# Kernel tuning notes

Hardware: AMD Instinct MI355X
Metric: run time of the kernel (lower is better)

## Reference

```python
import jax, jax.numpy as jnp
import numpy as np

N, E, D, L, BOT = 50000, 800000, 64, 5, 15
EPS = 1e-5  # BatchNorm eps (torch default)
GATE = 0.01


def _bn(x, g, b):
    # training-mode BatchNorm1d over the node (batch) axis, biased variance
    m = jnp.mean(x, axis=0)
    v = jnp.mean((x - m) ** 2, axis=0)
    return (x - m) * jax.lax.rsqrt(v + EPS) * g + b


def _adapter(x, w1, b1, w2, b2, g, b):
    # Linear(D->BOT) -> ReLU -> Linear(BOT->D) -> BatchNorm1d
    h = jax.nn.relu(x @ w1 + b1)
    return _bn(h @ w2 + b2, g, b)


def setup_inputs() -> dict:
    key = jax.random.key(0)
    ks = jax.random.split(key, 8)
    x = jax.random.normal(ks[0], (N, D), dtype=jnp.float32)
    edge_index = jax.random.randint(ks[1], (2, E), 0, N, dtype=jnp.int32)
    # per-layer conv Linear weights
    W = jax.random.normal(ks[2], (L, D, D), dtype=jnp.float32) * 0.05
    b = jnp.zeros((L, D), dtype=jnp.float32)
    # per-layer output BatchNorm
    bn_g = jnp.ones((L, D), dtype=jnp.float32)
    bn_b = jnp.zeros((L, D), dtype=jnp.float32)
    # adapter branches: [prompt_num=2, L, ...] (random init so grads are nontrivial)
    pw1 = jax.random.normal(ks[3], (2, L, D, BOT), dtype=jnp.float32) * 0.1
    pb1 = jnp.zeros((2, L, BOT), dtype=jnp.float32)
    pw2 = jax.random.normal(ks[4], (2, L, BOT, D), dtype=jnp.float32) * 0.1
    pb2 = jnp.zeros((2, L, D), dtype=jnp.float32)
    pbn_g = jnp.ones((2, L, D), dtype=jnp.float32)
    pbn_b = jnp.zeros((2, L, D), dtype=jnp.float32)
    gating = jnp.full((2, L, 1), GATE, dtype=jnp.float32)
    return dict(x=x, edge_index=edge_index, W=W, b=b, bn_g=bn_g, bn_b=bn_b,
                pw1=pw1, pb1=pb1, pw2=pw2, pb2=pb2, pbn_g=pbn_g, pbn_b=pbn_b,
                gating=gating)


def reference(x, edge_index, W, b, bn_g, bn_b, pw1, pb1, pw2, pb2, pbn_g, pbn_b, gating):
    src, dst = edge_index[0], edge_index[1]
    h = x
    for l in range(L):
        # mess: sum-aggregate neighbor features (scatter-add over dst)
        x_aggr = jax.ops.segment_sum(h[src], dst, num_segments=N)  # [N, D]
        # conv: Linear on aggregated messages
        h_mlp = x_aggr @ W[l] + b[l]
        hn = _bn(h_mlp, bn_g[l], bn_b[l])
        # adapter branch 0 on layer input, branch 1 on aggregated messages
        hn = hn + _adapter(h, pw1[0, l], pb1[0, l], pw2[0, l], pb2[0, l], pbn_g[0, l], pbn_b[0, l]) * gating[0, l]
        hn = hn + _adapter(x_aggr, pw1[1, l], pb1[1, l], pw2[1, l], pb2[1, l], pbn_g[1, l], pbn_b[1, l]) * gating[1, l]
        if l < L - 1:
            hn = jax.nn.relu(hn)
        # dropout with drop_ratio=0 is a no-op
        h = hn
    return h
```

## Files before the change

### kernel.cpp

```cpp
#include <hip/hip_runtime.h>

#define DIM 64
#define BOT 15
#define NLAYERS 5
#define BN_EPS 1e-5f
#define ROWS 64
#define ROWS_FB 32
#define BKT_SHIFT 8

__device__ inline void fma4(float4& acc, const float4& a, float s) {
    acc.x = fmaf(a.x, s, acc.x); acc.y = fmaf(a.y, s, acc.y);
    acc.z = fmaf(a.z, s, acc.z); acc.w = fmaf(a.w, s, acc.w);
}
__device__ inline void add4(float4& acc, const float4& a) {
    acc.x += a.x; acc.y += a.y; acc.z += a.z; acc.w += a.w;
}
__device__ inline void fma4sq(float4& acc, const float4& a) {
    acc.x = fmaf(a.x, a.x, acc.x); acc.y = fmaf(a.y, a.y, acc.y);
    acc.z = fmaf(a.z, a.z, acc.z); acc.w = fmaf(a.w, a.w, acc.w);
}
__device__ inline void wavered4(float4& v) {
    v.x += __shfl_xor(v.x, 16); v.y += __shfl_xor(v.y, 16);
    v.z += __shfl_xor(v.z, 16); v.w += __shfl_xor(v.w, 16);
    v.x += __shfl_xor(v.x, 32); v.y += __shfl_xor(v.y, 32);
    v.z += __shfl_xor(v.z, 32); v.w += __shfl_xor(v.w, 32);
}


__global__ __launch_bounds__(256) void hist_k(const int* __restrict__ dst,
                                              int* __restrict__ deg, int E) {
    int e = blockIdx.x * blockDim.x + threadIdx.x;
    if (e < E) atomicAdd(&deg[dst[e]], 1);
}

__global__ __launch_bounds__(1024) void scan_part_k(const int* __restrict__ deg,
                                                    int* __restrict__ excl,
                                                    int* __restrict__ bsum, int n) {
    __shared__ int buf[1024];
    int t = threadIdx.x;
    int idx = blockIdx.x * 1024 + t;
    int v = (idx < n) ? deg[idx] : 0;
    buf[t] = v;
    __syncthreads();
    for (int off = 1; off < 1024; off <<= 1) {
        int x = (t >= off) ? buf[t - off] : 0;
        __syncthreads();
        buf[t] += x;
        __syncthreads();
    }
    if (idx < n) excl[idx] = buf[t] - v;
    if (t == 0) bsum[blockIdx.x] = buf[1023];
}

__global__ __launch_bounds__(1024) void scan_top_k(const int* __restrict__ bsum,
                                                   int* __restrict__ boff, int nb,
                                                   int* __restrict__ row_ptr, int n) {
    __shared__ int buf[1024];
    int t = threadIdx.x;
    int v = (t < nb) ? bsum[t] : 0;
    buf[t] = v;
    __syncthreads();
    for (int off = 1; off < 1024; off <<= 1) {
        int x = (t >= off) ? buf[t - off] : 0;
        __syncthreads();
        buf[t] += x;
        __syncthreads();
    }
    if (t < nb) boff[t] = buf[t] - v;
    if (t == 1023) row_ptr[n] = buf[1023];
}

__global__ __launch_bounds__(256) void scan_add_k(int* __restrict__ row_ptr,
                                                  const int* __restrict__ boff,
                                                  int* __restrict__ deg,
                                                  int* __restrict__ bcur, int n) {
    int i = blockIdx.x * blockDim.x + threadIdx.x;
    if (i < n) {
        int v = row_ptr[i] + boff[i >> 10];
        row_ptr[i] = v;
        deg[i] = v;
        if ((i & 255) == 0) bcur[i >> BKT_SHIFT] = v;
    }
}

__global__ __launch_bounds__(256) void scatter_k(const int* __restrict__ src,
                                                 const int* __restrict__ dst,
                                                 int* __restrict__ cursor,
                                                 int* __restrict__ csr, int E) {
    int e = blockIdx.x * blockDim.x + threadIdx.x;
    if (e < E) {
        int p = atomicAdd(&cursor[dst[e]], 1);
        csr[p] = src[e];
    }
}

__global__ __launch_bounds__(256) void part_k(const int* __restrict__ src,
                                              const int* __restrict__ dst,
                                              int* __restrict__ bcur,
                                              int2* __restrict__ part, int E) {
    __shared__ int hist[256];
    __shared__ int cur[256];
    int t = threadIdx.x;
    int base = blockIdx.x * 2048;
    hist[t] = 0;
    __syncthreads();
    int2 ed[8];
    int bk[8];
    #pragma unroll
    for (int k = 0; k < 8; k++) {
        int i = base + k * 256 + t;
        if (i < E) {
            ed[k].x = src[i];
            ed[k].y = dst[i];
            bk[k] = ed[k].y >> BKT_SHIFT;
            atomicAdd(&hist[bk[k]], 1);
        } else bk[k] = -1;
    }
    __syncthreads();
    int h = hist[t];
    if (h > 0) cur[t] = atomicAdd(&bcur[t], h);
    __syncthreads();
    #pragma unroll
    for (int k = 0; k < 8; k++) {
        if (bk[k] >= 0) {
            int p = atomicAdd(&cur[bk[k]], 1);
            part[p] = ed[k];
        }
    }
}

__global__ __launch_bounds__(256) void bscat_k(const int2* __restrict__ part,
                                               const int* __restrict__ row_ptr,
                                               int* __restrict__ cursor,
                                               int* __restrict__ csr, int n) {
    int b = blockIdx.x;
    int lo = row_ptr[b << BKT_SHIFT];
    int hiN = (b + 1) << BKT_SHIFT;
    int hi = row_ptr[hiN < n ? hiN : n];
    for (int i = lo + (int)threadIdx.x; i < hi; i += 256) {
        int2 e = part[i];
        int p = atomicAdd(&cursor[e.y], 1);
        csr[p] = e.x;
    }
}


__global__ __launch_bounds__(256) void aggr_k(const float* __restrict__ h,
                                              const int* __restrict__ row_ptr,
                                              const int* __restrict__ csr,
                                              float* __restrict__ out, int n) {
    int gid = blockIdx.x * blockDim.x + threadIdx.x;
    int node = gid >> 6;
    int lane = threadIdx.x & 63;
    if (node >= n) return;
    int j = lane >> 4, q = lane & 15;
    int s = row_ptr[node], e = row_ptr[node + 1];
    float4 acc = {0.f, 0.f, 0.f, 0.f};
    #pragma unroll 4
    for (int i = s; i < e; i += 4) {
        int ii = i + j;
        if (ii < e) {
            int idx = csr[ii];
            float4 v = *(const float4*)&h[(size_t)idx * DIM + q * 4];
            add4(acc, v);
        }
    }
    wavered4(acc);
    if (lane < 16) *(float4*)&out[(size_t)node * DIM + q * 4] = acc;
}


__global__ __launch_bounds__(512, 4) void stats_k(
    const float* __restrict__ h, const float* __restrict__ aggr,
    const float* __restrict__ Wc, const float* __restrict__ bc,
    const float* __restrict__ p1a, const float* __restrict__ b1a,
    const float* __restrict__ p2a, const float* __restrict__ b2a,
    const float* __restrict__ p1b, const float* __restrict__ b1b,
    const float* __restrict__ p2b, const float* __restrict__ b2b,
    float* __restrict__ partials,
    float* __restrict__ yv, float* __restrict__ uv, float* __restrict__ vv,
    int n) {
    __shared__ float xa_s[ROWS][68];
    __shared__ float wc_s[64][64];
    __shared__ float p1t_s[2][15][68];
    __shared__ float p2_s[2][15][64];
    __shared__ float m_s[2][ROWS][17];
    __shared__ float red_s[6][8][64];

    int t = threadIdx.x;
    int rowBase = blockIdx.x * ROWS;

    #pragma unroll
    for (int i = 0; i < 2; i++) {
        int idx = t + i * 512;
        int r = idx >> 4, c4 = (idx & 15) * 4;
        int gr = rowBase + r;
        float4 va = {0.f, 0.f, 0.f, 0.f};
        if (gr < n) va = *(const float4*)&aggr[(size_t)gr * DIM + c4];
        *(float4*)&xa_s[r][c4] = va;
    }
    #pragma unroll
    for (int i = 0; i < 2; i++) {
        int idx = t + i * 512;
        int k = idx >> 4, c4 = (idx & 15) * 4;
        *(float4*)&wc_s[k][c4] = *(const float4*)&Wc[k * DIM + c4];
    }
    if (t < 240) {
        int m = t >> 4, c4 = (t & 15) * 4;
        *(float4*)&p2_s[0][m][c4] = *(const float4*)&p2a[m * DIM + c4];
        *(float4*)&p2_s[1][m][c4] = *(const float4*)&p2b[m * DIM + c4];
    }
    #pragma unroll
    for (int i = 0; i < 2; i++) {
        int idx = t + i * 512;
        if (idx < 960) {
            int k = idx / 15, m = idx % 15;
            p1t_s[0][m][k] = p1a[idx];
            p1t_s[1][m][k] = p1b[idx];
        }
    }
    __syncthreads();

    {
        int m = t & 15, r2 = t >> 4;
        if (m < 15) {
            #pragma unroll
            for (int half = 0; half < 2; half++) {
                int r = r2 + half * 32;
                int gr = rowBase + r;
                if (gr < n) {
                    float sA = b1a[m], sB = b1b[m];
                    const float4* hp = (const float4*)&h[(size_t)gr * DIM];
                    #pragma unroll 4
                    for (int kq = 0; kq < 16; kq++) {
                        float4 hv = hp[kq];
                        float4 av = *(const float4*)&xa_s[r][kq * 4];
                        float4 wA = *(const float4*)&p1t_s[0][m][kq * 4];
                        float4 wB = *(const float4*)&p1t_s[1][m][kq * 4];
                        sA = fmaf(hv.x, wA.x, sA); sA = fmaf(hv.y, wA.y, sA);
                        sA = fmaf(hv.z, wA.z, sA); sA = fmaf(hv.w, wA.w, sA);
                        sB = fmaf(av.x, wB.x, sB); sB = fmaf(av.y, wB.y, sB);
                        sB = fmaf(av.z, wB.z, sB); sB = fmaf(av.w, wB.w, sB);
                    }
                    m_s[0][r][m] = fmaxf(sA, 0.f);
                    m_s[1][r][m] = fmaxf(sB, 0.f);
                } else {
                    m_s[0][r][m] = 0.f;
                    m_s[1][r][m] = 0.f;
                }
            }
        }
    }
    __syncthreads();

    int cg = t & 15, rg = t >> 4;
    int c0 = cg * 4;
    int r0 = rg, r1 = rg + 32;

    float4 s0 = *(const float4*)&bc[c0];
    float4 s1 = s0;
    #pragma unroll 4
    for (int kq = 0; kq < 16; kq++) {
        float4 w0 = *(const float4*)&wc_s[kq * 4 + 0][c0];
        float4 w1 = *(const float4*)&wc_s[kq * 4 + 1][c0];
        float4 w2 = *(const float4*)&wc_s[kq * 4 + 2][c0];
        float4 w3 = *(const float4*)&wc_s[kq * 4 + 3][c0];
        float4 a0 = *(const float4*)&xa_s[r0][kq * 4];
        float4 a1 = *(const float4*)&xa_s[r1][kq * 4];
        fma4(s0, w0, a0.x); fma4(s0, w1, a0.y); fma4(s0, w2, a0.z); fma4(s0, w3, a0.w);
        fma4(s1, w0, a1.x); fma4(s1, w1, a1.y); fma4(s1, w2, a1.z); fma4(s1, w3, a1.w);
    }

    float4 u0 = *(const float4*)&b2a[c0];
    float4 u1 = u0;
    float4 v0 = *(const float4*)&b2b[c0];
    float4 v1 = v0;
    #pragma unroll 5
    for (int m = 0; m < BOT; m++) {
        float4 wa = *(const float4*)&p2_s[0][m][c0];
        float4 wb = *(const float4*)&p2_s[1][m][c0];
        float a0 = m_s[0][r0][m], a1 = m_s[0][r1][m];
        float b0 = m_s[1][r0][m], b1 = m_s[1][r1][m];
        fma4(u0, wa, a0); fma4(u1, wa, a1);
        fma4(v0, wb, b0); fma4(v1, wb, b1);
    }

    float4 sy = {0,0,0,0}, sy2 = {0,0,0,0};
    float4 su = {0,0,0,0}, su2 = {0,0,0,0};
    float4 sv = {0,0,0,0}, sv2 = {0,0,0,0};
    {
        int gr = rowBase + r0;
        if (gr < n) {
            size_t o = (size_t)gr * DIM + c0;
            *(float4*)&yv[o] = s0; *(float4*)&uv[o] = u0; *(float4*)&vv[o] = v0;
            add4(sy, s0); fma4sq(sy2, s0);
            add4(su, u0); fma4sq(su2, u0);
            add4(sv, v0); fma4sq(sv2, v0);
        }
        gr = rowBase + r1;
        if (gr < n) {
            size_t o = (size_t)gr * DIM + c0;
            *(float4*)&yv[o] = s1; *(float4*)&uv[o] = u1; *(float4*)&vv[o] = v1;
            add4(sy, s1); fma4sq(sy2, s1);
            add4(su, u1); fma4sq(su2, u1);
            add4(sv, v1); fma4sq(sv2, v1);
        }
    }

    wavered4(sy); wavered4(sy2);
    wavered4(su); wavered4(su2);
    wavered4(sv); wavered4(sv2);

    int wv = t >> 6, lane = t & 63;
    if (lane < 16) {
        *(float4*)&red_s[0][wv][c0] = sy;
        *(float4*)&red_s[1][wv][c0] = sy2;
        *(float4*)&red_s[2][wv][c0] = su;
        *(float4*)&red_s[3][wv][c0] = su2;
        *(float4*)&red_s[4][wv][c0] = sv;
        *(float4*)&red_s[5][wv][c0] = sv2;
    }
    __syncthreads();
    if (t < DIM) {
        #pragma unroll
        for (int j = 0; j < 6; j++) {
            float v = red_s[j][0][t] + red_s[j][1][t] + red_s[j][2][t] + red_s[j][3][t]
                    + red_s[j][4][t] + red_s[j][5][t] + red_s[j][6][t] + red_s[j][7][t];
            partials[((size_t)blockIdx.x * 6 + j) * DIM + t] = v;
        }
    }
}


template <int RELU>
__global__ __launch_bounds__(256) void apply_k(
    const float* __restrict__ yv, const float* __restrict__ uv,
    const float* __restrict__ vv, const float* __restrict__ ST,
    float* __restrict__ out, int n4) {
    int i = blockIdx.x * blockDim.x + threadIdx.x;
    if (i >= n4) return;
    int c4 = (i & 15) * 4;
    float4 S0 = *(const float4*)&ST[c4];
    float4 T0 = *(const float4*)&ST[64 + c4];
    float4 S1 = *(const float4*)&ST[128 + c4];
    float4 T1 = *(const float4*)&ST[192 + c4];
    float4 S2 = *(const float4*)&ST[256 + c4];
    float4 T2 = *(const float4*)&ST[320 + c4];
    float4 y = *(const float4*)&yv[(size_t)i * 4];
    float4 u = *(const float4*)&uv[(size_t)i * 4];
    float4 v = *(const float4*)&vv[(size_t)i * 4];
    float4 r;
    r.x = fmaf(y.x, S0.x, T0.x) + fmaf(u.x, S1.x, T1.x) + fmaf(v.x, S2.x, T2.x);
    r.y = fmaf(y.y, S0.y, T0.y) + fmaf(u.y, S1.y, T1.y) + fmaf(v.y, S2.y, T2.y);
    r.z = fmaf(y.z, S0.z, T0.z) + fmaf(u.z, S1.z, T1.z) + fmaf(v.z, S2.z, T2.z);
    r.w = fmaf(y.w, S0.w, T0.w) + fmaf(u.w, S1.w, T1.w) + fmaf(v.w, S2.w, T2.w);
    if (RELU) {
        r.x = fmaxf(r.x, 0.f); r.y = fmaxf(r.y, 0.f);
        r.z = fmaxf(r.z, 0.f); r.w = fmaxf(r.w, 0.f);
    }
    *(float4*)&out[(size_t)i * 4] = r;
}


template <int MODE>
__global__ __launch_bounds__(256) void layer_k(
    const float* __restrict__ h, const float* __restrict__ aggr,
    const float* __restrict__ Wc, const float* __restrict__ bc,
    const float* __restrict__ p1a, const float* __restrict__ b1a,
    const float* __restrict__ p2a, const float* __restrict__ b2a,
    const float* __restrict__ p1b, const float* __restrict__ b1b,
    const float* __restrict__ p2b, const float* __restrict__ b2b,
    float* __restrict__ partials, const float* __restrict__ ST,
    float* __restrict__ hout, int n) {
    __shared__ float xh[ROWS_FB][DIM + 1];
    __shared__ float xa[ROWS_FB][DIM + 1];
    __shared__ float m0[ROWS_FB][17];
    __shared__ float m1[ROWS_FB][17];
    __shared__ float red[6][4][DIM];

    int t = threadIdx.x;
    int rowBase = blockIdx.x * ROWS_FB;

    #pragma unroll
    for (int i = 0; i < (ROWS_FB * DIM) / 256; i++) {
        int idx = t + i * 256;
        int r = idx >> 6, c = idx & 63;
        int gr = rowBase + r;
        float vh = 0.f, va = 0.f;
        if (gr < n) { vh = h[(size_t)gr * DIM + c]; va = aggr[(size_t)gr * DIM + c]; }
        xh[r][c] = vh;
        xa[r][c] = va;
    }
    __syncthreads();

    {
        int r = t >> 3, sub = t & 7;
        #pragma unroll
        for (int half = 0; half < 2; half++) {
            int m = sub + half * 8;
            if (m < BOT) {
                float s0 = b1a[m], s1 = b1b[m];
                #pragma unroll
                for (int k = 0; k < DIM; k++) {
                    s0 = fmaf(xh[r][k], p1a[k * BOT + m], s0);
                    s1 = fmaf(xa[r][k], p1b[k * BOT + m], s1);
                }
                m0[r][m] = fmaxf(s0, 0.f);
                m1[r][m] = fmaxf(s1, 0.f);
            }
        }
    }
    __syncthreads();

    int col = t & 63;
    int rg = t >> 6;
    float sums[6] = {0.f, 0.f, 0.f, 0.f, 0.f, 0.f};
    float S0 = 0, T0 = 0, S1 = 0, T1 = 0, S2 = 0, T2 = 0;
    if (MODE != 0) {
        S0 = ST[col];        T0 = ST[64 + col];
        S1 = ST[128 + col];  T1 = ST[192 + col];
        S2 = ST[256 + col];  T2 = ST[320 + col];
    }
    #pragma unroll
    for (int i = 0; i < ROWS_FB / 4; i++) {
        int r = rg + i * 4;
        int gr = rowBase + r;
        float s = bc[col];
        #pragma unroll
        for (int k = 0; k < DIM; k++) s = fmaf(xa[r][k], Wc[k * DIM + col], s);
        float u = b2a[col];
        #pragma unroll
        for (int m = 0; m < BOT; m++) u = fmaf(m0[r][m], p2a[m * DIM + col], u);
        float v = b2b[col];
        #pragma unroll
        for (int m = 0; m < BOT; m++) v = fmaf(m1[r][m], p2b[m * DIM + col], v);
        if (MODE == 0) {
            if (gr < n) {
                sums[0] += s; sums[1] += s * s;
                sums[2] += u; sums[3] += u * u;
                sums[4] += v; sums[5] += v * v;
            }
        } else {
            float r0 = fmaf(s, S0, T0) + fmaf(u, S1, T1) + fmaf(v, S2, T2);
            if (MODE == 2) r0 = fmaxf(r0, 0.f);
            if (gr < n) hout[(size_t)gr * DIM + col] = r0;
        }
    }

    if (MODE == 0) {
        #pragma unroll
        for (int j = 0; j < 6; j++) red[j][rg][col] = sums[j];
        __syncthreads();
        if (t < DIM) {
            #pragma unroll
            for (int j = 0; j < 6; j++) {
                float v = red[j][0][t] + red[j][1][t] + red[j][2][t] + red[j][3][t];
                partials[((size_t)blockIdx.x * 6 + j) * DIM + t] = v;
            }
        }
    }
}


__global__ __launch_bounds__(256) void reduce_fold_k(
    const float* __restrict__ partials, int nb, int n,
    const float* __restrict__ bn_g, const float* __restrict__ bn_b,
    const float* __restrict__ pg0, const float* __restrict__ pb0,
    const float* __restrict__ pg1, const float* __restrict__ pb1,
    const float* __restrict__ gating, int l, float* __restrict__ ST) {
    __shared__ double red[6][256];
    int col = blockIdx.x;
    int t = threadIdx.x;
    double acc[6] = {0, 0, 0, 0, 0, 0};
    for (int b = t; b < nb; b += 256) {
        const float* p = partials + (size_t)b * 6 * DIM + col;
        #pragma unroll
        for (int j = 0; j < 6; j++) acc[j] += (double)p[j * DIM];
    }
    #pragma unroll
    for (int j = 0; j < 6; j++) red[j][t] = acc[j];
    __syncthreads();
    for (int off = 128; off > 0; off >>= 1) {
        if (t < off) {
            #pragma unroll
            for (int j = 0; j < 6; j++) red[j][t] += red[j][t + off];
        }
        __syncthreads();
    }
    if (t < 3) {
        int stat = t;
        float mean = (float)(red[2 * stat][0] / (double)n);
        float var = (float)(red[2 * stat + 1][0] / (double)n) - mean * mean;
        float rstd = rsqrtf(fmaxf(var, 0.f) + BN_EPS);
        float g, bb, gate;
        if (stat == 0)      { g = bn_g[col]; bb = bn_b[col]; gate = 1.f; }
        else if (stat == 1) { g = pg0[col];  bb = pb0[col];  gate = gating[0 * NLAYERS + l]; }
        else                { g = pg1[col];  bb = pb1[col];  gate = gating[1 * NLAYERS + l]; }
        float S = g * rstd * gate;
        float T = (bb - mean * g * rstd) * gate;
        ST[stat * 128 + col] = S;
        ST[stat * 128 + 64 + col] = T;
    }
}


static inline char* bump(char*& p, size_t bytes) {
    char* r = p;
    p += (bytes + 255) & ~(size_t)255;
    return r;
}

extern "C" void kernel_launch(void* const* d_in, const int* in_sizes, int n_in,
                              void* d_out, int out_size, void* d_ws, size_t ws_size,
                              hipStream_t stream) {
    const float* x      = (const float*)d_in[0];
    const int*   ei     = (const int*)d_in[1];
    const float* W      = (const float*)d_in[2];
    const float* bconv  = (const float*)d_in[3];
    const float* bn_g   = (const float*)d_in[4];
    const float* bn_b   = (const float*)d_in[5];
    const float* pw1    = (const float*)d_in[6];
    const float* pb1    = (const float*)d_in[7];
    const float* pw2    = (const float*)d_in[8];
    const float* pb2    = (const float*)d_in[9];
    const float* pbn_g  = (const float*)d_in[10];
    const float* pbn_b  = (const float*)d_in[11];
    const float* gating = (const float*)d_in[12];

    int n = in_sizes[0] / DIM;
    int E = in_sizes[1] / 2;
    int nbS  = (n + ROWS - 1) / ROWS;
    int nbFB = (n + ROWS_FB - 1) / ROWS_FB;
    int nb1024 = (n + 1023) / 1024;
    int nbkt = (n + 255) >> BKT_SHIFT;
    size_t n64b = (size_t)n * DIM * sizeof(float);

    char* p = (char*)d_ws;
    float* h_ws     = (float*)bump(p, n64b);
    float* partials = (float*)bump(p, (size_t)nbFB * 6 * DIM * sizeof(float));
    float* ST       = (float*)bump(p, 6 * 128 * sizeof(float));
    int*   bsum     = (int*)bump(p, (size_t)nb1024 * sizeof(int));
    int*   boff     = (int*)bump(p, (size_t)nb1024 * sizeof(int));
    int*   bcur     = (int*)bump(p, 257 * sizeof(int));
    int*   deg      = (int*)bump(p, (size_t)n * sizeof(int));
    int*   row_ptr  = (int*)bump(p, (size_t)(n + 1) * sizeof(int));
    int*   csr      = (int*)bump(p, (size_t)E * sizeof(int));
    float* aggr     = (float*)bump(p, n64b);
    float* yv = (float*)bump(p, n64b);
    float* uv = (float*)bump(p, n64b);
    float* vv = (float*)bump(p, n64b);
    bool fast = ((size_t)(p - (char*)d_ws) <= ws_size);
    int2* part = (int2*)yv;

    const int* esrc = ei;
    const int* edst = ei + E;

    hipMemsetAsync(deg, 0, (size_t)n * sizeof(int), stream);
    hist_k<<<(E + 255) / 256, 256, 0, stream>>>(edst, deg, E);
    scan_part_k<<<nb1024, 1024, 0, stream>>>(deg, row_ptr, bsum, n);
    scan_top_k<<<1, 1024, 0, stream>>>(bsum, boff, nb1024, row_ptr, n);
    scan_add_k<<<(n + 255) / 256, 256, 0, stream>>>(row_ptr, boff, deg, bcur, n);
    if (fast) {
        part_k<<<(E + 2047) / 2048, 256, 0, stream>>>(esrc, edst, bcur, part, E);
        bscat_k<<<nbkt, 256, 0, stream>>>(part, row_ptr, deg, csr, n);
    } else {
        scatter_k<<<(E + 255) / 256, 256, 0, stream>>>(esrc, edst, deg, csr, E);
    }

    for (int l = 0; l < NLAYERS; l++) {
        const float* Wl  = W     + (size_t)l * DIM * DIM;
        const float* bl  = bconv + (size_t)l * DIM;
        const float* bgl = bn_g  + (size_t)l * DIM;
        const float* bbl = bn_b  + (size_t)l * DIM;
        const float* p1a = pw1 + ((size_t)0 * NLAYERS + l) * DIM * BOT;
        const float* p1b = pw1 + ((size_t)1 * NLAYERS + l) * DIM * BOT;
        const float* b1a = pb1 + ((size_t)0 * NLAYERS + l) * BOT;
        const float* b1b = pb1 + ((size_t)1 * NLAYERS + l) * BOT;
        const float* p2a = pw2 + ((size_t)0 * NLAYERS + l) * BOT * DIM;
        const float* p2b = pw2 + ((size_t)1 * NLAYERS + l) * BOT * DIM;
        const float* b2a = pb2 + ((size_t)0 * NLAYERS + l) * DIM;
        const float* b2b = pb2 + ((size_t)1 * NLAYERS + l) * DIM;
        const float* g0  = pbn_g + ((size_t)0 * NLAYERS + l) * DIM;
        const float* g1  = pbn_g + ((size_t)1 * NLAYERS + l) * DIM;
        const float* be0 = pbn_b + ((size_t)0 * NLAYERS + l) * DIM;
        const float* be1 = pbn_b + ((size_t)1 * NLAYERS + l) * DIM;

        const float* hin = (l == 0) ? x : h_ws;

        aggr_k<<<(n + 3) / 4, 256, 0, stream>>>(hin, row_ptr, csr, aggr, n);

        if (fast) {
            stats_k<<<nbS, 512, 0, stream>>>(
                hin, aggr, Wl, bl, p1a, b1a, p2a, b2a,
                p1b, b1b, p2b, b2b, partials, yv, uv, vv, n);

            reduce_fold_k<<<DIM, 256, 0, stream>>>(partials, nbS, n, bgl, bbl,
                                                   g0, be0, g1, be1, gating, l, ST);

            int n4 = n * (DIM / 4);
            float* outp = (l < NLAYERS - 1) ? h_ws : (float*)d_out;
            if (l < NLAYERS - 1)
                apply_k<1><<<(n4 + 255) / 256, 256, 0, stream>>>(yv, uv, vv, ST, outp, n4);
            else
                apply_k<0><<<(n4 + 255) / 256, 256, 0, stream>>>(yv, uv, vv, ST, outp, n4);
        } else {
            layer_k<0><<<nbFB, 256, 0, stream>>>(
                hin, aggr, Wl, bl, p1a, b1a, p2a, b2a, p1b, b1b, p2b, b2b,
                partials, nullptr, nullptr, n);

            reduce_fold_k<<<DIM, 256, 0, stream>>>(partials, nbFB, n, bgl, bbl,
                                                   g0, be0, g1, be1, gating, l, ST);

            if (l < NLAYERS - 1) {
                layer_k<2><<<nbFB, 256, 0, stream>>>(
                    hin, aggr, Wl, bl, p1a, b1a, p2a, b2a, p1b, b1b, p2b, b2b,
                    nullptr, ST, h_ws, n);
            } else {
                layer_k<1><<<nbFB, 256, 0, stream>>>(
                    hin, aggr, Wl, bl, p1a, b1a, p2a, b2a, p1b, b1b, p2b, b2b,
                    nullptr, ST, (float*)d_out, n);
            }
        }
    }
}
```

Measured before the change: 488.8 us.

## Replace per-block BN partials and reduce kernel with striped atomics folded into apply

stats_k now atomically adds its per-block BatchNorm sums into a small striped global accumulator (4 stripes per layer) instead of writing per-block partials. The separate reduce_fold launch is removed, and each apply_k block recomputes the scale/shift from the stripes in shared memory. This saves one kernel launch and the serial partial reduction per layer. In exchange it adds float atomic contention on few addresses, redundant fold work in every apply block, and a memset of the accumulators. It also computes variance as E[x^2]-mean^2, where the reference subtracts the mean first, which may lose precision.

```diff
diff --git a/kernel.cpp b/kernel.cpp
--- a/kernel.cpp
+++ b/kernel.cpp
@@ -7,6 +7,7 @@
 #define ROWS 64
 #define ROWS_FB 32
 #define BKT_SHIFT 8
+#define NSTRIPE 4
 
 __device__ inline void fma4(float4& acc, const float4& a, float s) {
     acc.x = fmaf(a.x, s, acc.x); acc.y = fmaf(a.y, s, acc.y);
@@ -177,7 +178,7 @@
     const float* __restrict__ p2a, const float* __restrict__ b2a,
     const float* __restrict__ p1b, const float* __restrict__ b1b,
     const float* __restrict__ p2b, const float* __restrict__ b2b,
-    float* __restrict__ partials,
+    float* __restrict__ gsum,
     float* __restrict__ yv, float* __restrict__ uv, float* __restrict__ vv,
     int n) {
     __shared__ float xa_s[ROWS][68];
@@ -322,11 +323,12 @@
     }
     __syncthreads();
     if (t < DIM) {
+        float* gs = gsum + (size_t)(blockIdx.x & (NSTRIPE - 1)) * 6 * DIM;
         #pragma unroll
         for (int j = 0; j < 6; j++) {
             float v = red_s[j][0][t] + red_s[j][1][t] + red_s[j][2][t] + red_s[j][3][t]
                     + red_s[j][4][t] + red_s[j][5][t] + red_s[j][6][t] + red_s[j][7][t];
-            partials[((size_t)blockIdx.x * 6 + j) * DIM + t] = v;
+            atomicAdd(&gs[j * DIM + t], v);
         }
     }
 }
@@ -335,17 +337,43 @@
 template <int RELU>
 __global__ __launch_bounds__(256) void apply_k(
     const float* __restrict__ yv, const float* __restrict__ uv,
-    const float* __restrict__ vv, const float* __restrict__ ST,
+    const float* __restrict__ vv, const float* __restrict__ gsum,
+    const float* __restrict__ bn_g, const float* __restrict__ bn_b,
+    const float* __restrict__ pg0, const float* __restrict__ pb0,
+    const float* __restrict__ pg1, const float* __restrict__ pb1,
+    const float* __restrict__ gating, int l, int n,
     float* __restrict__ out, int n4) {
-    int i = blockIdx.x * blockDim.x + threadIdx.x;
+    __shared__ float STs[6][64];
+    int t = threadIdx.x;
+    if (t < 192) {
+        int stat = t >> 6, c = t & 63;
+        float s1 = 0.f, s2 = 0.f;
+        #pragma unroll
+        for (int k = 0; k < NSTRIPE; k++) {
+            const float* gs = gsum + (size_t)k * 6 * DIM;
+            s1 += gs[(2 * stat) * DIM + c];
+            s2 += gs[(2 * stat + 1) * DIM + c];
+        }
+        float mean = s1 / (float)n;
+        float var = s2 / (float)n - mean * mean;
+        float rstd = rsqrtf(fmaxf(var, 0.f) + BN_EPS);
+        float g, bb, gate;
+        if (stat == 0)      { g = bn_g[c]; bb = bn_b[c]; gate = 1.f; }
+        else if (stat == 1) { g = pg0[c];  bb = pb0[c];  gate = gating[0 * NLAYERS + l]; }
+        else                { g = pg1[c];  bb = pb1[c];  gate = gating[1 * NLAYERS + l]; }
+        STs[2 * stat][c] = g * rstd * gate;
+        STs[2 * stat + 1][c] = (bb - mean * g * rstd) * gate;
+    }
+    __syncthreads();
+    int i = blockIdx.x * blockDim.x + t;
     if (i >= n4) return;
     int c4 = (i & 15) * 4;
-    float4 S0 = *(const float4*)&ST[c4];
-    float4 T0 = *(const float4*)&ST[64 + c4];
-    float4 S1 = *(const float4*)&ST[128 + c4];
-    float4 T1 = *(const float4*)&ST[192 + c4];
-    float4 S2 = *(const float4*)&ST[256 + c4];
-    float4 T2 = *(const float4*)&ST[320 + c4];
+    float4 S0 = *(const float4*)&STs[0][c4];
+    float4 T0 = *(const float4*)&STs[1][c4];
+    float4 S1 = *(const float4*)&STs[2][c4];
+    float4 T1 = *(const float4*)&STs[3][c4];
+    float4 S2 = *(const float4*)&STs[4][c4];
+    float4 T2 = *(const float4*)&STs[5][c4];
     float4 y = *(const float4*)&yv[(size_t)i * 4];
     float4 u = *(const float4*)&uv[(size_t)i * 4];
     float4 v = *(const float4*)&vv[(size_t)i * 4];
@@ -539,6 +567,7 @@
     float* h_ws     = (float*)bump(p, n64b);
     float* partials = (float*)bump(p, (size_t)nbFB * 6 * DIM * sizeof(float));
     float* ST       = (float*)bump(p, 6 * 128 * sizeof(float));
+    float* gsum     = (float*)bump(p, (size_t)NLAYERS * NSTRIPE * 6 * DIM * sizeof(float));
     int*   bsum     = (int*)bump(p, (size_t)nb1024 * sizeof(int));
     int*   boff     = (int*)bump(p, (size_t)nb1024 * sizeof(int));
     int*   bcur     = (int*)bump(p, 257 * sizeof(int));
@@ -556,6 +585,7 @@
     const int* edst = ei + E;
 
     hipMemsetAsync(deg, 0, (size_t)n * sizeof(int), stream);
+    hipMemsetAsync(gsum, 0, (size_t)NLAYERS * NSTRIPE * 6 * DIM * sizeof(float), stream);
     hist_k<<<(E + 255) / 256, 256, 0, stream>>>(edst, deg, E);
     scan_part_k<<<nb1024, 1024, 0, stream>>>(deg, row_ptr, bsum, n);
     scan_top_k<<<1, 1024, 0, stream>>>(bsum, boff, nb1024, row_ptr, n);
@@ -586,23 +616,23 @@
         const float* be1 = pbn_b + ((size_t)1 * NLAYERS + l) * DIM;
 
         const float* hin = (l == 0) ? x : h_ws;
+        float* gsl = gsum + (size_t)l * NSTRIPE * 6 * DIM;
 
         aggr_k<<<(n + 3) / 4, 256, 0, stream>>>(hin, row_ptr, csr, aggr, n);
 
         if (fast) {
             stats_k<<<nbS, 512, 0, stream>>>(
                 hin, aggr, Wl, bl, p1a, b1a, p2a, b2a,
-                p1b, b1b, p2b, b2b, partials, yv, uv, vv, n);
-
-            reduce_fold_k<<<DIM, 256, 0, stream>>>(partials, nbS, n, bgl, bbl,
-                                                   g0, be0, g1, be1, gating, l, ST);
+                p1b, b1b, p2b, b2b, gsl, yv, uv, vv, n);
 
             int n4 = n * (DIM / 4);
             float* outp = (l < NLAYERS - 1) ? h_ws : (float*)d_out;
             if (l < NLAYERS - 1)
-                apply_k<1><<<(n4 + 255) / 256, 256, 0, stream>>>(yv, uv, vv, ST, outp, n4);
+                apply_k<1><<<(n4 + 255) / 256, 256, 0, stream>>>(
+                    yv, uv, vv, gsl, bgl, bbl, g0, be0, g1, be1, gating, l, n, outp, n4);
             else
-                apply_k<0><<<(n4 + 255) / 256, 256, 0, stream>>>(yv, uv, vv, ST, outp, n4);
+                apply_k<0><<<(n4 + 255) / 256, 256, 0, stream>>>(
+                    yv, uv, vv, gsl, bgl, bbl, g0, be0, g1, be1, gating, l, n, outp, n4);
         } else {
             layer_k<0><<<nbFB, 256, 0, stream>>>(
                 hin, aggr, Wl, bl, p1a, b1a, p2a, b2a, p1b, b1b, p2b, b2b,
```

New measurement: 458.2 us. 6.3% less time.
